# Kernel tuning notes

Measured on AMD Instinct MI355X. Metric: run time of the kernel, lower is better.

Reference implementation:

```python
import jax, jax.numpy as jnp
import numpy as np

NEG_BIG = -9e15
LEAKY_SLOPE = 0.01  # nn.LeakyReLU default

N, IN_DIM, HIDDEN_DIM, OUT_DIM = 16384, 512, 256, 128


def setup_inputs() -> dict:
    key = jax.random.key(0)
    ks = jax.random.split(key, 6)
    # He-ish init scaled like torch Linear defaults (uniform +-1/sqrt(fan_in))
    def lin_init(k, fan_in, fan_out):
        kw, kb = jax.random.split(k)
        bound = 1.0 / np.sqrt(fan_in)
        W = jax.random.uniform(kw, (fan_in, fan_out), jnp.float32, -bound, bound)
        b = jax.random.uniform(kb, (fan_out,), jnp.float32, -bound, bound)
        return W, b
    W1, b1 = lin_init(ks[0], IN_DIM, HIDDEN_DIM)
    W2, b2 = lin_init(ks[1], HIDDEN_DIM, OUT_DIM)
    x = jax.random.normal(ks[2], (N, IN_DIM), jnp.float32)
    return {
        "x": x,
        "g": 0,  # unused graph arg in the executed forward path
        "W1": W1, "b1": b1,
        "W2": W2, "b2": b2,
        "alpha": jnp.array([0.1], jnp.float32),
        "beta": jnp.array([0.9], jnp.float32),
    }


def _sim_agg(x):
    # adj: [N, N] dense similarity
    adj = jnp.matmul(x, x.T)
    a = jnp.where(adj > 0, adj, jnp.float32(NEG_BIG))
    sim1 = jax.nn.softmax(a, axis=1)
    return jnp.matmul(sim1, x)


def reference(x, g, W1, b1, W2, b2, alpha, beta):
    # dropout is inactive in eval mode (F.dropout with training=False)
    h = jnp.matmul(x, W1) + b1
    h = jnp.where(h >= 0, h, LEAKY_SLOPE * h)  # LeakyReLU
    h = jnp.matmul(h, W2) + b2                 # [N, out_dim]
    out = alpha * _sim_agg(h) + beta * h
    return jax.nn.log_softmax(out, axis=1)
```

## Files before the change

### kernel.cpp

```cpp
#include <hip/hip_runtime.h>
#include <hip/hip_bf16.h>

typedef __bf16 bf16_t;
typedef __bf16 bf16x8 __attribute__((ext_vector_type(8)));
typedef __bf16 bf16x4 __attribute__((ext_vector_type(4)));
typedef __bf16 bf16x2 __attribute__((ext_vector_type(2)));
typedef float f32x4 __attribute__((ext_vector_type(4)));
typedef float f32x2 __attribute__((ext_vector_type(2)));
typedef unsigned short u16;

#define NROWS 16384
#define KDIM  512
#define HID   256
#define ODIM  128
#define KS    8

__device__ __forceinline__ f32x4 mfma16(bf16x8 a, bf16x8 b, f32x4 c) {
  return __builtin_amdgcn_mfma_f32_16x16x32_bf16(a, b, c, 0, 0, 0);
}

__device__ __forceinline__ void dma16(const void* g, void* l) {
  __builtin_amdgcn_global_load_lds(
      (const __attribute__((address_space(1))) unsigned int*)g,
      (__attribute__((address_space(3))) unsigned int*)l, 16, 0, 0);
}

__global__ __launch_bounds__(256) void prep(const float* __restrict__ x,
                                            const float* __restrict__ W1,
                                            const float* __restrict__ W2,
                                            bf16_t* __restrict__ xb,
                                            bf16_t* __restrict__ W1T,
                                            bf16_t* __restrict__ W2T) {
  int t = blockIdx.x * 256 + threadIdx.x;
  int stride = gridDim.x * 256;
  for (int e = t; e < NROWS * KDIM / 4; e += stride) {
    f32x4 v = *(const f32x4*)(x + (size_t)e * 4);
    bf16x4 pk;
    pk[0] = (bf16_t)v[0]; pk[1] = (bf16_t)v[1];
    pk[2] = (bf16_t)v[2]; pk[3] = (bf16_t)v[3];
    *(bf16x4*)(xb + (size_t)e * 4) = pk;
  }
  for (int e = t; e < HID * KDIM; e += stride) {
    int n = e >> 9, k = e & 511;
    W1T[e] = (bf16_t)W1[k * HID + n];
  }
  for (int e = t; e < ODIM * HID; e += stride) {
    int n = e >> 8, k = e & 255;
    W2T[e] = (bf16_t)W2[k * ODIM + n];
  }
}

__global__ __launch_bounds__(256) void gemm1(const bf16_t* __restrict__ xb,
                                             const bf16_t* __restrict__ W1T,
                                             const float* __restrict__ b1,
                                             bf16_t* __restrict__ h1) {
  __shared__ u16 As[128 * 40];
  __shared__ u16 Bs[64 * 40];
  int tid = threadIdx.x;
  int lane = tid & 63, w = tid >> 6;
  int r = lane & 15, q = lane >> 4;
  int wm = w & 1, wn = w >> 1;
  int mbase = blockIdx.x * 128, nbase = blockIdx.y * 64;

  f32x4 acc[4][2];
#pragma unroll
  for (int ms = 0; ms < 4; ms++)
#pragma unroll
    for (int ns = 0; ns < 2; ns++) acc[ms][ns] = (f32x4){0.f, 0.f, 0.f, 0.f};

  for (int kb = 0; kb < KDIM; kb += 32) {
#pragma unroll
    for (int i = 0; i < 2; i++) {
      int g = tid + 256 * i;
      int rr = g >> 2, c = (g & 3) * 8;
      *(bf16x8*)&As[rr * 40 + c] =
          *(const bf16x8*)(xb + (size_t)(mbase + rr) * KDIM + kb + c);
    }
    {
      int rr = tid >> 2, c = (tid & 3) * 8;
      *(bf16x8*)&Bs[rr * 40 + c] =
          *(const bf16x8*)(W1T + (size_t)(nbase + rr) * KDIM + kb + c);
    }
    __syncthreads();
    bf16x8 af[4], bfr[2];
#pragma unroll
    for (int ms = 0; ms < 4; ms++)
      af[ms] = *(bf16x8*)&As[(wm * 64 + ms * 16 + r) * 40 + q * 8];
#pragma unroll
    for (int ns = 0; ns < 2; ns++)
      bfr[ns] = *(bf16x8*)&Bs[(wn * 32 + ns * 16 + r) * 40 + q * 8];
#pragma unroll
    for (int ms = 0; ms < 4; ms++)
#pragma unroll
      for (int ns = 0; ns < 2; ns++)
        acc[ms][ns] = mfma16(af[ms], bfr[ns], acc[ms][ns]);
    __syncthreads();
  }
#pragma unroll
  for (int ns = 0; ns < 2; ns++) {
    int col = nbase + wn * 32 + ns * 16 + r;
    float bias = b1[col];
#pragma unroll
    for (int ms = 0; ms < 4; ms++) {
      int row0 = mbase + wm * 64 + ms * 16 + q * 4;
#pragma unroll
      for (int reg = 0; reg < 4; reg++) {
        float v = acc[ms][ns][reg] + bias;
        v = v >= 0.f ? v : 0.01f * v;
        h1[(size_t)(row0 + reg) * HID + col] = (bf16_t)v;
      }
    }
  }
}

__global__ __launch_bounds__(256) void gemm2(const bf16_t* __restrict__ h1,
                                             const bf16_t* __restrict__ W2T,
                                             const float* __restrict__ b2,
                                             bf16_t* __restrict__ hb,
                                             bf16_t* __restrict__ hT) {
  __shared__ u16 As[128 * 40];
  __shared__ u16 Bs[64 * 40];
  int tid = threadIdx.x;
  int lane = tid & 63, w = tid >> 6;
  int r = lane & 15, q = lane >> 4;
  int wm = w & 1, wn = w >> 1;
  int mbase = blockIdx.x * 128, nbase = blockIdx.y * 64;

  f32x4 acc[4][2];
#pragma unroll
  for (int ms = 0; ms < 4; ms++)
#pragma unroll
    for (int ns = 0; ns < 2; ns++) acc[ms][ns] = (f32x4){0.f, 0.f, 0.f, 0.f};

  for (int kb = 0; kb < HID; kb += 32) {
#pragma unroll
    for (int i = 0; i < 2; i++) {
      int g = tid + 256 * i;
      int rr = g >> 2, c = (g & 3) * 8;
      *(bf16x8*)&As[rr * 40 + c] =
          *(const bf16x8*)(h1 + (size_t)(mbase + rr) * HID + kb + c);
    }
    {
      int rr = tid >> 2, c = (tid & 3) * 8;
      *(bf16x8*)&Bs[rr * 40 + c] =
          *(const bf16x8*)(W2T + (size_t)(nbase + rr) * HID + kb + c);
    }
    __syncthreads();
    bf16x8 af[4], bfr[2];
#pragma unroll
    for (int ms = 0; ms < 4; ms++)
      af[ms] = *(bf16x8*)&As[(wm * 64 + ms * 16 + r) * 40 + q * 8];
#pragma unroll
    for (int ns = 0; ns < 2; ns++)
      bfr[ns] = *(bf16x8*)&Bs[(wn * 32 + ns * 16 + r) * 40 + q * 8];
#pragma unroll
    for (int ms = 0; ms < 4; ms++)
#pragma unroll
      for (int ns = 0; ns < 2; ns++)
        acc[ms][ns] = mfma16(af[ms], bfr[ns], acc[ms][ns]);
    __syncthreads();
  }
#pragma unroll
  for (int ns = 0; ns < 2; ns++) {
    int col = nbase + wn * 32 + ns * 16 + r;
    float bias = b2[col];
#pragma unroll
    for (int ms = 0; ms < 4; ms++) {
      int row0 = mbase + wm * 64 + ms * 16 + q * 4;
      bf16x4 pk;
#pragma unroll
      for (int reg = 0; reg < 4; reg++) {
        float v = acc[ms][ns][reg] + bias;
        hb[(size_t)(row0 + reg) * ODIM + col] = (bf16_t)v;
        pk[reg] = (bf16_t)v;
      }
      *(bf16x4*)(hT + (size_t)col * NROWS + row0) = pk;
    }
  }
}

__global__ __launch_bounds__(256, 4) void flash(const bf16_t* __restrict__ hb,
                                                const bf16_t* __restrict__ hT,
                                                bf16_t* __restrict__ OpA,
                                                bf16_t* __restrict__ OpB,
                                                float* __restrict__ Ml) {
  __shared__ __align__(16) u16 KA[8 * 512];
  __shared__ __align__(16) u16 KT[2][8 * 512];
  __shared__ __align__(16) u16 Pm[4 * 32 * 40];

  int tid = threadIdx.x;
  int lane = tid & 63, w = tid >> 6;
  int r = lane & 15, q = lane >> 4;
  int ksplit = blockIdx.x >> 7;
  int qtile = blockIdx.x & 127;
  int qbase = qtile * 128 + w * 32;
  int kbase = ksplit * (NROWS / KS);
  const int niter = (NROWS / KS) / 32;

  const char* gbase;
  size_t jmul;
  int ginc;
  u16* dbase;
  if (w < 2) {
    gbase = (const char*)(hb + (size_t)(kbase + w * 16 + r) * ODIM + q * 8);
    jmul = 32 * 2;
    ginc = 32 * ODIM * 2;
    dbase = KA + w * 4 * 512;
  } else {
    gbase = (const char*)(hT + (size_t)((w - 2) * 64 + r) * NROWS + kbase + q * 8);
    jmul = (size_t)16 * NROWS * 2;
    ginc = 32 * 2;
    dbase = KT[0] + (w - 2) * 4 * 512;
  }

  bf16x8 qf[2][4];
#pragma unroll
  for (int qt = 0; qt < 2; qt++) {
    int qrow = qbase + qt * 16 + r;
#pragma unroll
    for (int kk = 0; kk < 4; kk++)
      qf[qt][kk] = *(const bf16x8*)(hb + (size_t)qrow * ODIM + kk * 32 + q * 8);
  }

  f32x4 oa[8][2];
#pragma unroll
  for (int m8 = 0; m8 < 8; m8++)
#pragma unroll
    for (int qt = 0; qt < 2; qt++) oa[m8][qt] = (f32x4){0.f, 0.f, 0.f, 0.f};
  float m_run[2] = {0.f, 0.f}, l_run[2] = {0.f, 0.f};

#pragma unroll
  for (int j = 0; j < 4; j++) dma16(gbase + j * jmul, dbase + j * 512);
  gbase += ginc;

  for (int it = 0; it < niter; it++) {
    __syncthreads();

    f32x4 s[2][2];
#pragma unroll
    for (int mt = 0; mt < 2; mt++)
#pragma unroll
      for (int qt = 0; qt < 2; qt++) s[mt][qt] = (f32x4){0.f, 0.f, 0.f, 0.f};
#pragma unroll
    for (int mt = 0; mt < 2; mt++)
#pragma unroll
      for (int kk = 0; kk < 4; kk++) {
        bf16x8 af = *(bf16x8*)&KA[(mt * 4 + kk) * 512 + lane * 8];
        s[mt][0] = mfma16(af, qf[0][kk], s[mt][0]);
        s[mt][1] = mfma16(af, qf[1][kk], s[mt][1]);
      }
    __syncthreads();

    if (it + 1 < niter) {
      u16* d = dbase;
      if (w >= 2) d += ((it + 1) & 1) * 4096;
#pragma unroll
      for (int j = 0; j < 4; j++) dma16(gbase + j * jmul, d + j * 512);
      gbase += ginc;
    }

    float mx[2];
#pragma unroll
    for (int qt = 0; qt < 2; qt++) {
      float m = m_run[qt];
#pragma unroll
      for (int mt = 0; mt < 2; mt++)
#pragma unroll
        for (int reg = 0; reg < 4; reg++) {
          float v = s[mt][qt][reg];
          m = v > 0.f ? fmaxf(m, v) : m;
        }
      m = fmaxf(m, __shfl_xor(m, 16, 64));
      m = fmaxf(m, __shfl_xor(m, 32, 64));
      mx[qt] = m;
    }
    if (__any(mx[0] > m_run[0] || mx[1] > m_run[1])) {
      float sc0 = __expf(m_run[0] - mx[0]);
      float sc1 = __expf(m_run[1] - mx[1]);
      m_run[0] = mx[0]; m_run[1] = mx[1];
      l_run[0] *= sc0; l_run[1] *= sc1;
#pragma unroll
      for (int m8 = 0; m8 < 8; m8++)
#pragma unroll
        for (int reg = 0; reg < 4; reg++) {
          oa[m8][0][reg] *= sc0;
          oa[m8][1][reg] *= sc1;
        }
    }
#pragma unroll
    for (int qt = 0; qt < 2; qt++) {
      float rs = 0.f;
      bf16x4 pk[2];
#pragma unroll
      for (int mt = 0; mt < 2; mt++)
#pragma unroll
        for (int reg = 0; reg < 4; reg++) {
          float v = s[mt][qt][reg];
          float p = v > 0.f ? __expf(v - m_run[qt]) : 0.f;
          rs += p;
          pk[mt][reg] = (bf16_t)p;
        }
      rs += __shfl_xor(rs, 16, 64);
      rs += __shfl_xor(rs, 32, 64);
      l_run[qt] += rs;
#pragma unroll
      for (int mt = 0; mt < 2; mt++)
        *(bf16x4*)&Pm[w * 1280 + (qt * 16 + r) * 40 + mt * 16 + q * 4] = pk[mt];
    }

    bf16x8 pf0 = *(bf16x8*)&Pm[w * 1280 + r * 40 + q * 8];
    bf16x8 pf1 = *(bf16x8*)&Pm[w * 1280 + (16 + r) * 40 + q * 8];
    const u16* kt = KT[it & 1];
#pragma unroll
    for (int m8 = 0; m8 < 8; m8++) {
      bf16x8 af = *(bf16x8*)&kt[m8 * 512 + lane * 8];
      oa[m8][0] = mfma16(af, pf0, oa[m8][0]);
      oa[m8][1] = mfma16(af, pf1, oa[m8][1]);
    }
  }

  bf16_t* op = ksplit < 6 ? OpA + (size_t)ksplit * NROWS * ODIM
                          : OpB + (size_t)(ksplit - 6) * NROWS * ODIM;
#pragma unroll
  for (int qt = 0; qt < 2; qt++) {
    int row = qbase + qt * 16 + r;
#pragma unroll
    for (int m8 = 0; m8 < 8; m8++) {
      bf16x4 pk;
#pragma unroll
      for (int reg = 0; reg < 4; reg++) pk[reg] = (bf16_t)oa[m8][qt][reg];
      *(bf16x4*)(op + (size_t)row * ODIM + m8 * 16 + q * 4) = pk;
    }
    if (q == 0) {
      Ml[(ksplit * NROWS + row) * 2 + 0] = m_run[qt];
      Ml[(ksplit * NROWS + row) * 2 + 1] = l_run[qt];
    }
  }
}

__global__ __launch_bounds__(256) void merge_ls(const bf16_t* __restrict__ OpA,
                                                const bf16_t* __restrict__ OpB,
                                                const float* __restrict__ Ml,
                                                const bf16_t* __restrict__ hbf,
                                                const float* __restrict__ alpha_p,
                                                const float* __restrict__ beta_p,
                                                float* __restrict__ out) {
  int tid = threadIdx.x, lane = tid & 63, w = tid >> 6;
  float al = alpha_p[0], be = beta_p[0];
  for (int i = 0; i < 8; i++) {
    int row = blockIdx.x * 32 + w * 8 + i;
    float mk[KS], lk[KS], ak[KS];
    float M = 0.f;
#pragma unroll
    for (int ksp = 0; ksp < KS; ksp++) {
      mk[ksp] = Ml[(ksp * NROWS + row) * 2 + 0];
      lk[ksp] = Ml[(ksp * NROWS + row) * 2 + 1];
      M = fmaxf(M, mk[ksp]);
    }
    float lt = 0.f;
#pragma unroll
    for (int ksp = 0; ksp < KS; ksp++) {
      ak[ksp] = __expf(mk[ksp] - M);
      lt += lk[ksp] * ak[ksp];
    }
    float inv = al / lt;
    int d0 = lane * 2;
    float a0 = 0.f, a1 = 0.f;
#pragma unroll
    for (int ksp = 0; ksp < KS; ksp++) {
      const bf16_t* op = ksp < 6 ? OpA + (size_t)ksp * NROWS * ODIM
                                 : OpB + (size_t)(ksp - 6) * NROWS * ODIM;
      bf16x2 v = *(const bf16x2*)(op + (size_t)row * ODIM + d0);
      a0 += ak[ksp] * (float)v[0];
      a1 += ak[ksp] * (float)v[1];
    }
    bf16x2 hv = *(const bf16x2*)(hbf + (size_t)row * ODIM + d0);
    float v0 = inv * a0 + be * (float)hv[0];
    float v1 = inv * a1 + be * (float)hv[1];
    float mxv = fmaxf(v0, v1);
#pragma unroll
    for (int off = 1; off < 64; off <<= 1) mxv = fmaxf(mxv, __shfl_xor(mxv, off, 64));
    float se = __expf(v0 - mxv) + __expf(v1 - mxv);
#pragma unroll
    for (int off = 1; off < 64; off <<= 1) se += __shfl_xor(se, off, 64);
    float lz = mxv + __logf(se);
    f32x2 st = {v0 - lz, v1 - lz};
    *(f32x2*)(out + (size_t)row * ODIM + d0) = st;
  }
}

extern "C" void kernel_launch(void* const* d_in, const int* in_sizes, int n_in,
                              void* d_out, int out_size, void* d_ws,
                              size_t ws_size, hipStream_t stream) {
  const float* x     = (const float*)d_in[0];
  const float* W1    = (const float*)d_in[2];
  const float* b1    = (const float*)d_in[3];
  const float* W2    = (const float*)d_in[4];
  const float* b2    = (const float*)d_in[5];
  const float* alpha = (const float*)d_in[6];
  const float* beta  = (const float*)d_in[7];

  char* ws = (char*)d_ws;
  bf16_t* xb  = (bf16_t*)(ws + 0);
  bf16_t* W1T = (bf16_t*)(ws + 16777216);
  bf16_t* W2T = (bf16_t*)(ws + 17039360);
  bf16_t* h1  = (bf16_t*)(ws + 17104896);
  bf16_t* hbf = (bf16_t*)(ws + 25493504);
  bf16_t* hT  = (bf16_t*)(ws + 29687808);
  float*  Ml  = (float*)(ws + 33882112);
  bf16_t* OpB = (bf16_t*)(ws + 34930688);
  bf16_t* OpA = (bf16_t*)(ws + 0);
  float* outp = (float*)d_out;

  prep<<<1024, 256, 0, stream>>>(x, W1, W2, xb, W1T, W2T);
  gemm1<<<dim3(128, 4), 256, 0, stream>>>(xb, W1T, b1, h1);
  gemm2<<<dim3(128, 2), 256, 0, stream>>>(h1, W2T, b2, hbf, hT);
  flash<<<128 * KS, 256, 0, stream>>>(hbf, hT, OpA, OpB, Ml);
  merge_ls<<<512, 256, 0, stream>>>(OpA, OpB, Ml, hbf, alpha, beta, outp);
}
```

Before: 365.9 us.

## Keep softmax P in registers via permlane swaps, lazy rescale, exp2, setprio

```diff
diff --git a/kernel.cpp b/kernel.cpp
--- a/kernel.cpp
+++ b/kernel.cpp
@@ -8,12 +8,14 @@
 typedef float f32x4 __attribute__((ext_vector_type(4)));
 typedef float f32x2 __attribute__((ext_vector_type(2)));
 typedef unsigned short u16;
+typedef unsigned int u32;
 
 #define NROWS 16384
 #define KDIM  512
 #define HID   256
 #define ODIM  128
 #define KS    8
+#define LOG2E 1.44269504f
 
 __device__ __forceinline__ f32x4 mfma16(bf16x8 a, bf16x8 b, f32x4 c) {
   return __builtin_amdgcn_mfma_f32_16x16x32_bf16(a, b, c, 0, 0, 0);
@@ -23,6 +25,20 @@
   __builtin_amdgcn_global_load_lds(
       (const __attribute__((address_space(1))) unsigned int*)g,
       (__attribute__((address_space(3))) unsigned int*)l, 16, 0, 0);
+}
+
+__device__ __forceinline__ void pl32swap(u32& a, u32& b) {
+  asm("v_permlane32_swap_b32 %0, %1" : "+v"(a), "+v"(b));
+}
+__device__ __forceinline__ void pl16swap(u32& a, u32& b) {
+  asm("v_permlane16_swap_b32 %0, %1" : "+v"(a), "+v"(b));
+}
+
+__device__ __forceinline__ u32 pack2(float a, float b) {
+  bf16x2 t;
+  t[0] = (bf16_t)a;
+  t[1] = (bf16_t)b;
+  return __builtin_bit_cast(u32, t);
 }
 
 __global__ __launch_bounds__(256) void prep(const float* __restrict__ x,
@@ -186,7 +202,6 @@
                                                 float* __restrict__ Ml) {
   __shared__ __align__(16) u16 KA[8 * 512];
   __shared__ __align__(16) u16 KT[2][8 * 512];
-  __shared__ __align__(16) u16 Pm[4 * 32 * 40];
 
   int tid = threadIdx.x;
   int lane = tid & 63, w = tid >> 6;
@@ -228,6 +243,7 @@
 #pragma unroll
     for (int qt = 0; qt < 2; qt++) oa[m8][qt] = (f32x4){0.f, 0.f, 0.f, 0.f};
   float m_run[2] = {0.f, 0.f}, l_run[2] = {0.f, 0.f};
+  float mlog[2] = {0.f, 0.f};
 
 #pragma unroll
   for (int j = 0; j < 4; j++) dma16(gbase + j * jmul, dbase + j * 512);
@@ -241,6 +257,7 @@
     for (int mt = 0; mt < 2; mt++)
 #pragma unroll
       for (int qt = 0; qt < 2; qt++) s[mt][qt] = (f32x4){0.f, 0.f, 0.f, 0.f};
+    __builtin_amdgcn_s_setprio(1);
 #pragma unroll
     for (int mt = 0; mt < 2; mt++)
 #pragma unroll
@@ -249,6 +266,7 @@
         s[mt][0] = mfma16(af, qf[0][kk], s[mt][0]);
         s[mt][1] = mfma16(af, qf[1][kk], s[mt][1]);
       }
+    __builtin_amdgcn_s_setprio(0);
     __syncthreads();
 
     if (it + 1 < niter) {
@@ -266,18 +284,16 @@
 #pragma unroll
       for (int mt = 0; mt < 2; mt++)
 #pragma unroll
-        for (int reg = 0; reg < 4; reg++) {
-          float v = s[mt][qt][reg];
-          m = v > 0.f ? fmaxf(m, v) : m;
-        }
+        for (int reg = 0; reg < 4; reg++) m = fmaxf(m, s[mt][qt][reg]);
       m = fmaxf(m, __shfl_xor(m, 16, 64));
       m = fmaxf(m, __shfl_xor(m, 32, 64));
       mx[qt] = m;
     }
-    if (__any(mx[0] > m_run[0] || mx[1] > m_run[1])) {
-      float sc0 = __expf(m_run[0] - mx[0]);
-      float sc1 = __expf(m_run[1] - mx[1]);
+    if (__any(mx[0] > m_run[0] + 8.f || mx[1] > m_run[1] + 8.f)) {
+      float sc0 = __builtin_amdgcn_exp2f((m_run[0] - mx[0]) * LOG2E);
+      float sc1 = __builtin_amdgcn_exp2f((m_run[1] - mx[1]) * LOG2E);
       m_run[0] = mx[0]; m_run[1] = mx[1];
+      mlog[0] = mx[0] * LOG2E; mlog[1] = mx[1] * LOG2E;
       l_run[0] *= sc0; l_run[1] *= sc1;
 #pragma unroll
       for (int m8 = 0; m8 < 8; m8++)
@@ -287,36 +303,44 @@
           oa[m8][1][reg] *= sc1;
         }
     }
+
+    union W8 { u32 wrd[4]; bf16x8 v; } pfq[2];
 #pragma unroll
     for (int qt = 0; qt < 2; qt++) {
       float rs = 0.f;
-      bf16x4 pk[2];
+      float pv[2][4];
 #pragma unroll
       for (int mt = 0; mt < 2; mt++)
 #pragma unroll
         for (int reg = 0; reg < 4; reg++) {
           float v = s[mt][qt][reg];
-          float p = v > 0.f ? __expf(v - m_run[qt]) : 0.f;
+          float p = __builtin_amdgcn_exp2f(fmaf(v, LOG2E, -mlog[qt]));
+          p = v > 0.f ? p : 0.f;
           rs += p;
-          pk[mt][reg] = (bf16_t)p;
+          pv[mt][reg] = p;
         }
       rs += __shfl_xor(rs, 16, 64);
       rs += __shfl_xor(rs, 32, 64);
       l_run[qt] += rs;
-#pragma unroll
-      for (int mt = 0; mt < 2; mt++)
-        *(bf16x4*)&Pm[w * 1280 + (qt * 16 + r) * 40 + mt * 16 + q * 4] = pk[mt];
-    }
-
-    bf16x8 pf0 = *(bf16x8*)&Pm[w * 1280 + r * 40 + q * 8];
-    bf16x8 pf1 = *(bf16x8*)&Pm[w * 1280 + (16 + r) * 40 + q * 8];
+      u32 A = pack2(pv[0][0], pv[0][1]);
+      u32 B = pack2(pv[0][2], pv[0][3]);
+      u32 C = pack2(pv[1][0], pv[1][1]);
+      u32 D = pack2(pv[1][2], pv[1][3]);
+      pl32swap(A, C); pl16swap(A, C);
+      pl32swap(B, D); pl16swap(B, D);
+      pfq[qt].wrd[0] = A; pfq[qt].wrd[1] = B;
+      pfq[qt].wrd[2] = C; pfq[qt].wrd[3] = D;
+    }
+
     const u16* kt = KT[it & 1];
+    __builtin_amdgcn_s_setprio(1);
 #pragma unroll
     for (int m8 = 0; m8 < 8; m8++) {
       bf16x8 af = *(bf16x8*)&kt[m8 * 512 + lane * 8];
-      oa[m8][0] = mfma16(af, pf0, oa[m8][0]);
-      oa[m8][1] = mfma16(af, pf1, oa[m8][1]);
-    }
+      oa[m8][0] = mfma16(af, pfq[0].v, oa[m8][0]);
+      oa[m8][1] = mfma16(af, pfq[1].v, oa[m8][1]);
+    }
+    __builtin_amdgcn_s_setprio(0);
   }
 
   bf16_t* op = ksplit < 6 ? OpA + (size_t)ksplit * NROWS * ODIM
```

After: 414.8 us. +13.4%, slower.
